# Kernel tuning notes

Hardware: AMD Instinct MI355X
Metric: run time of the kernel (lower is better)

The kernel has to match this reference:

```python
import jax, jax.numpy as jnp
import numpy as np

N_NODES = 100000
N_EDGES = 1600000
IN_DIM = 128      # 1 (degree) + 127 (raw feat)
HID = 128
N_GRAPHS = 100


def setup_inputs() -> dict:
    key = jax.random.key(0)
    ks = jax.random.split(key, 16)
    feat = jax.random.normal(ks[0], (N_NODES, IN_DIM - 1), dtype=jnp.float32)
    src = jax.random.randint(ks[1], (N_EDGES,), 0, N_NODES, dtype=jnp.int32)
    dst = jax.random.randint(ks[2], (N_EDGES,), 0, N_NODES, dtype=jnp.int32)
    graph_ids = jnp.sort(jax.random.randint(ks[3], (N_NODES,), 0, N_GRAPHS, dtype=jnp.int32))
    s = 1.0 / np.sqrt(IN_DIM)
    W0 = jax.random.uniform(ks[4], (HID, IN_DIM), jnp.float32, -s, s)
    b0 = jax.random.uniform(ks[5], (HID,), jnp.float32, -s, s)
    s = 1.0 / np.sqrt(HID)
    W1 = jax.random.uniform(ks[6], (HID, HID), jnp.float32, -s, s)
    b1 = jax.random.uniform(ks[7], (HID,), jnp.float32, -s, s)
    W2 = jax.random.uniform(ks[8], (HID, HID), jnp.float32, -s, s)
    b2 = jax.random.uniform(ks[9], (HID,), jnp.float32, -s, s)
    Wc1 = jax.random.uniform(ks[10], (HID, HID), jnp.float32, -s, s)
    bc1 = jax.random.uniform(ks[11], (HID,), jnp.float32, -s, s)
    Wc2 = jax.random.uniform(ks[12], (1, HID), jnp.float32, -s, s)
    bc2 = jax.random.uniform(ks[13], (1,), jnp.float32, -s, s)
    return {"feat": feat, "src": src, "dst": dst, "graph_ids": graph_ids,
            "num_graphs": N_GRAPHS,
            "W0": W0, "b0": b0, "W1": W1, "b1": b1, "W2": W2, "b2": b2,
            "Wc1": Wc1, "bc1": bc1, "Wc2": Wc2, "bc2": bc2}


def _gcn_layer(h, src, dst, deg, W, b):
    # mean over in-neighbor messages; zero-in-degree nodes keep old h (DGL reduce never fires)
    n = h.shape[0]
    summed = jax.ops.segment_sum(h[src], dst, num_segments=n)  # [N, d]
    mean = summed / jnp.maximum(deg, 1.0)[:, None]
    agg = jnp.where((deg > 0)[:, None], mean, h)
    return jax.nn.relu(agg @ W.T + b)


def reference(feat, src, dst, graph_ids, num_graphs,
              W0, b0, W1, b1, W2, b2, Wc1, bc1, Wc2, bc2):
    n = feat.shape[0]
    deg = jax.ops.segment_sum(jnp.ones(src.shape[0], jnp.float32), dst, num_segments=n)  # in-degrees
    h = jnp.concatenate([deg[:, None], feat], axis=-1)  # [N, IN_DIM]
    for W, b in ((W0, b0), (W1, b1), (W2, b2)):
        h = _gcn_layer(h, src, dst, deg, W, b)
    # dgl.mean_nodes: per-graph mean of node features
    counts = jax.ops.segment_sum(jnp.ones(n, jnp.float32), graph_ids, num_segments=num_graphs)
    hg = jax.ops.segment_sum(h, graph_ids, num_segments=num_graphs) / jnp.maximum(counts, 1.0)[:, None]
    # faithful: classify1 applied twice, no activation (F.relu was passed as bias flag)
    hg = hg @ Wc1.T + bc1
    hg = hg @ Wc1.T + bc1
    hg = hg @ Wc2.T + bc2
    return hg  # [num_graphs, 1]
```

## Files before the change

### kernel.cpp

```cpp
#include <hip/hip_runtime.h>
#include <hip/hip_bf16.h>

#define HID 128
#define NRAW 127
#define BSH 8
#define BNODES 256
#define EW 2048


typedef __attribute__((ext_vector_type(8))) short short8;
typedef __attribute__((ext_vector_type(4))) float floatx4;
typedef __attribute__((ext_vector_type(2))) float floatx2;

__device__ inline unsigned pack_bf2(float x, float y) {
    unsigned bx = __float_as_uint(x);
    unsigned by = __float_as_uint(y);
    bx += 0x7fffu + ((bx >> 16) & 1u);
    by += 0x7fffu + ((by >> 16) & 1u);
    return (bx >> 16) | (by & 0xffff0000u);
}
__device__ inline float bf_lo(unsigned u) { return __uint_as_float(u << 16); }
__device__ inline float bf_hi(unsigned u) { return __uint_as_float(u & 0xffff0000u); }


__global__ void init_kernel(const float* __restrict__ W0, const float* __restrict__ W1,
                            const float* __restrict__ W2, const float* __restrict__ Wc1,
                            unsigned* __restrict__ O0, unsigned* __restrict__ O1,
                            unsigned* __restrict__ O2, float* __restrict__ Wc1p,
                            int* __restrict__ gbucket, float* __restrict__ hg,
                            float* __restrict__ counts,
                            unsigned* __restrict__ h8a, unsigned* __restrict__ h8b,
                            int G, int N) {
    int id = blockIdx.x * blockDim.x + threadIdx.x;
    if (id < 512) gbucket[id] = 0;
    if (id < G * HID) hg[id] = 0.f;
    if (id < G) counts[id] = 0.f;
    if (id < 32) {
        h8a[(size_t)N * 32 + id] = 0u;
        h8b[(size_t)N * 32 + id] = 0u;
    }
    if (id < 16384) {
        int t = id >> 7, p = id & 127;
        Wc1p[id] = Wc1[t * 128 + ((p & 7) * 16 + (p >> 3))];
    }
    if (id < 3 * 8192) {
        int sel = id >> 13, l = id & 8191;
        const float* W = sel == 0 ? W0 : (sel == 1 ? W1 : W2);
        unsigned* O = sel == 0 ? O0 : (sel == 1 ? O1 : O2);
        int o = l >> 6, pp = (l & 63) * 2;
        int k0 = (pp & 7) * 16 + (pp >> 3);
        int k1 = ((pp + 1) & 7) * 16 + ((pp + 1) >> 3);
        O[l] = pack_bf2(W[o * 128 + k0], W[o * 128 + k1]);
    }
}


__global__ __launch_bounds__(256) void bucket_count_kernel(const int* __restrict__ dst,
                                                           int* __restrict__ gbucket,
                                                           int E, int NB) {
    __shared__ int hist[512];
    int t = threadIdx.x;
    for (int b = t; b < NB; b += 256) hist[b] = 0;
    __syncthreads();
    int base = blockIdx.x * 4096;
    #pragma unroll
    for (int j = 0; j < 16; ++j) {
        int e = base + j * 256 + t;
        if (e < E) atomicAdd(&hist[dst[e] >> BSH], 1);
    }
    __syncthreads();
    for (int b = t; b < NB; b += 256) {
        int v = hist[b];
        if (v) atomicAdd(&gbucket[b], v);
    }
}

__global__ void bucket_scan_kernel(const int* __restrict__ gbucket, int* __restrict__ bstart,
                                   int* __restrict__ gcur, int NB, int E) {
    __shared__ int sm[512];
    int t = threadIdx.x;
    int v = (t < NB) ? gbucket[t] : 0;
    sm[t] = v;
    __syncthreads();
    for (int off = 1; off < 512; off <<= 1) {
        int add = (t >= off) ? sm[t - off] : 0;
        __syncthreads();
        sm[t] += add;
        __syncthreads();
    }
    if (t < NB) {
        int ex = sm[t] - v;
        bstart[t] = ex;
        gcur[t] = ex;
    }
    if (t == 0) bstart[NB] = E;
}

__global__ __launch_bounds__(256) void bucket_scatter_kernel(const int* __restrict__ src,
                                                             const int* __restrict__ dst,
                                                             int* __restrict__ gcur,
                                                             unsigned* __restrict__ staging,
                                                             int E, int NB) {
    __shared__ int hist[512];
    __shared__ int base[512];
    int t = threadIdx.x;
    for (int b = t; b < NB; b += 256) hist[b] = 0;
    __syncthreads();
    int s[16], d[16], r[16];
    int e0 = blockIdx.x * 4096;
    #pragma unroll
    for (int j = 0; j < 16; ++j) {
        int e = e0 + j * 256 + t;
        if (e < E) {
            s[j] = src[e];
            d[j] = dst[e];
            r[j] = atomicAdd(&hist[d[j] >> BSH], 1);
        } else d[j] = -1;
    }
    __syncthreads();
    for (int b = t; b < NB; b += 256) {
        int v = hist[b];
        base[b] = v ? atomicAdd(&gcur[b], v) : 0;
    }
    __syncthreads();
    #pragma unroll
    for (int j = 0; j < 16; ++j) {
        if (d[j] >= 0) {
            int b = d[j] >> BSH;
            staging[base[b] + r[j]] = ((unsigned)s[j] << 8) | ((unsigned)d[j] & 255u);
        }
    }
}

__global__ __launch_bounds__(256) void csr_build_kernel(const unsigned* __restrict__ staging,
                                                        const int* __restrict__ bstart,
                                                        int* __restrict__ rp, int* __restrict__ csr,
                                                        float* __restrict__ degf,
                                                        int N, int E, int NB) {
    __shared__ int hist[256];
    __shared__ int sm[256];
    __shared__ int excl[256];
    __shared__ int cnt[256];
    int t = threadIdx.x;
    int b = blockIdx.x;
    int nbase = b << BSH;
    int s0 = bstart[b], e1 = bstart[b + 1];
    hist[t] = 0;
    __syncthreads();
    for (int i = s0 + t; i < e1; i += 256) {
        unsigned p = staging[i];
        atomicAdd(&hist[p & (BNODES - 1)], 1);
    }
    __syncthreads();
    int h = hist[t];
    sm[t] = h;
    __syncthreads();
    for (int off = 1; off < 256; off <<= 1) {
        int add = (t >= off) ? sm[t - off] : 0;
        __syncthreads();
        sm[t] += add;
        __syncthreads();
    }
    excl[t] = sm[t] - h;
    cnt[t] = 0;
    int n = nbase + t;
    if (n < N) {
        rp[n] = s0 + (sm[t] - h);
        degf[n] = (float)h;
    }
    if (b == NB - 1 && t == 0) {
        rp[N] = E;
        degf[N] = 0.f;
    }
    __syncthreads();
    for (int i = s0 + t; i < e1; i += 256) {
        unsigned p = staging[i];
        int dl = p & (BNODES - 1);
        int pos = s0 + excl[dl] + atomicAdd(&cnt[dl], 1);
        csr[pos] = (int)(p >> 8);
    }
}


__global__ __launch_bounds__(256) void build_h0_kernel(const float* __restrict__ feat,
                                                       unsigned* __restrict__ h8, int N) {
    __shared__ float lf[8 * NRAW];
    int t = threadIdx.x;
    int n0 = blockIdx.x * 8;
    int nrows = min(8, N - n0);
    int total = nrows * NRAW;
    for (int j = t; j < total; j += 256) lf[j] = feat[(size_t)n0 * NRAW + j];
    __syncthreads();
    int n = t >> 5, c = t & 31;
    if (n < nrows) {
        const float* fr = lf + n * NRAW;
        int base = c >> 1, hb = (c & 1) * 4;
        float f[4];
        #pragma unroll
        for (int j = 0; j < 4; ++j) {
            int l = (hb + j) * 16 + base;
            f[j] = (l == 0) ? 0.f : fr[l - 1];
        }
        unsigned w = __builtin_amdgcn_cvt_pk_fp8_f32(f[0], f[1], 0, false);
        w = __builtin_amdgcn_cvt_pk_fp8_f32(f[2], f[3], w, true);
        h8[(size_t)(n0 + n) * 32 + c] = w;
    }
}


__global__ __launch_bounds__(256, 4) void gcn_fused_kernel(const unsigned* __restrict__ h8,
                                                           unsigned* __restrict__ out8,
                                                           unsigned* __restrict__ outb,
                                                           const unsigned* __restrict__ Wb,
                                                           const float* __restrict__ bias,
                                                           const int* __restrict__ rp,
                                                           const int* __restrict__ csr,
                                                           const float* __restrict__ degf,
                                                           int col0fix, int N) {
    __shared__ unsigned Al[32 * 64];
    __shared__ unsigned CsS[32 * 64];
    int* sIdx = (int*)CsS;
    int t = threadIdx.x;
    int wv = t >> 6, lane = t & 63;
    int grp = lane >> 3;
    int cc4 = lane & 7;
    int n0 = blockIdx.x * 32;
    int g32 = wv * 8 + grp;
    int i = n0 + g32;
    const char* hbase = (const char*)h8;
    unsigned c16 = (unsigned)cc4 * 16u;

    int start = 0, end = 0;
    if (i < N) { start = rp[i]; end = rp[i + 1]; }
    int deg = end - start;
    int nEnd = min(n0 + 32, N);
    int s0 = rp[n0];
    int e1 = rp[nEnd];

    floatx2 a0 = {0.f, 0.f}, a1 = {0.f, 0.f}, a2 = {0.f, 0.f}, a3 = {0.f, 0.f};
    floatx2 a4 = {0.f, 0.f}, a5 = {0.f, 0.f}, a6 = {0.f, 0.f}, a7 = {0.f, 0.f};
    float dsum = 0.f;

    #define GATH4(ii) (*(const uint4*)(hbase + (((unsigned)(ii) << 7) + c16)))
    #define ACC4(vv) do { \
        a0 += __builtin_amdgcn_cvt_pk_f32_fp8((vv).x, false); \
        a1 += __builtin_amdgcn_cvt_pk_f32_fp8((vv).x, true);  \
        a2 += __builtin_amdgcn_cvt_pk_f32_fp8((vv).y, false); \
        a3 += __builtin_amdgcn_cvt_pk_f32_fp8((vv).y, true);  \
        a4 += __builtin_amdgcn_cvt_pk_f32_fp8((vv).z, false); \
        a5 += __builtin_amdgcn_cvt_pk_f32_fp8((vv).z, true);  \
        a6 += __builtin_amdgcn_cvt_pk_f32_fp8((vv).w, false); \
        a7 += __builtin_amdgcn_cvt_pk_f32_fp8((vv).w, true);  \
    } while (0)

    for (int w0 = s0; w0 < e1; w0 += EW) {
        if (w0 > s0) __syncthreads();
        int wcnt = min(EW, e1 - w0);
        for (int j = t; j < wcnt; j += 256) sIdx[j] = csr[w0 + j];
        __syncthreads();
        int p  = max(start, w0) - w0;
        int pe = min(end, w0 + wcnt) - w0;
        for (; p + 4 <= pe; p += 4) {
            int iA = sIdx[p], iB = sIdx[p + 1], iC = sIdx[p + 2], iD = sIdx[p + 3];
            uint4 vA = GATH4(iA), vB = GATH4(iB), vC = GATH4(iC), vD = GATH4(iD);
            if (col0fix && cc4 == 0)
                dsum += degf[iA] + degf[iB] + degf[iC] + degf[iD];
            ACC4(vA); ACC4(vB); ACC4(vC); ACC4(vD);
        }
        for (; p + 2 <= pe; p += 2) {
            int iA = sIdx[p], iB = sIdx[p + 1];
            uint4 vA = GATH4(iA), vB = GATH4(iB);
            if (col0fix && cc4 == 0) dsum += degf[iA] + degf[iB];
            ACC4(vA); ACC4(vB);
        }
        for (; p < pe; ++p) {
            int iA = sIdx[p];
            uint4 vA = GATH4(iA);
            if (col0fix && cc4 == 0) dsum += degf[iA];
            ACC4(vA);
        }
    }

    if (i < N) {
        float inv;
        if (deg == 0) {
            uint4 v = GATH4(i);
            ACC4(v);
            inv = 1.f;
        } else {
            if (col0fix && cc4 == 0) a0[0] = dsum;
            inv = 1.f / (float)deg;
        }
        uint4 r0, r1;
        r0.x = pack_bf2(a0[0] * inv, a0[1] * inv);
        r0.y = pack_bf2(a1[0] * inv, a1[1] * inv);
        r0.z = pack_bf2(a2[0] * inv, a2[1] * inv);
        r0.w = pack_bf2(a3[0] * inv, a3[1] * inv);
        r1.x = pack_bf2(a4[0] * inv, a4[1] * inv);
        r1.y = pack_bf2(a5[0] * inv, a5[1] * inv);
        r1.z = pack_bf2(a6[0] * inv, a6[1] * inv);
        r1.w = pack_bf2(a7[0] * inv, a7[1] * inv);
        int gr0 = 2 * cc4, gr1 = 2 * cc4 + 1;
        *(uint4*)&Al[(g32 * 16 + (gr0 ^ (g32 & 7))) * 4] = r0;
        *(uint4*)&Al[(g32 * 16 + (gr1 ^ (g32 & 7))) * 4] = r1;
    }
    __syncthreads();

    {
        int rh = wv & 1, cq = wv >> 1;
        int m = lane & 15, q = lane >> 4;
        int r = rh * 16 + m;
        floatx4 acc0 = (floatx4)(0.f), acc1 = (floatx4)(0.f);
        floatx4 acc2 = (floatx4)(0.f), acc3 = (floatx4)(0.f);
        #pragma unroll
        for (int kt = 0; kt < 4; ++kt) {
            short8 af = *(const short8*)&Al[(r * 16 + ((kt * 4 + q) ^ (m & 7))) * 4];
            short8 b0 = *(const short8*)&Wb[((cq * 4 + 0) * 16 + m) * 64 + kt * 16 + q * 4];
            short8 b1 = *(const short8*)&Wb[((cq * 4 + 1) * 16 + m) * 64 + kt * 16 + q * 4];
            short8 b2 = *(const short8*)&Wb[((cq * 4 + 2) * 16 + m) * 64 + kt * 16 + q * 4];
            short8 b3 = *(const short8*)&Wb[((cq * 4 + 3) * 16 + m) * 64 + kt * 16 + q * 4];
            acc0 = __builtin_amdgcn_mfma_f32_16x16x32_bf16(af, b0, acc0, 0, 0, 0);
            acc1 = __builtin_amdgcn_mfma_f32_16x16x32_bf16(af, b1, acc1, 0, 0, 0);
            acc2 = __builtin_amdgcn_mfma_f32_16x16x32_bf16(af, b2, acc2, 0, 0, 0);
            acc3 = __builtin_amdgcn_mfma_f32_16x16x32_bf16(af, b3, acc3, 0, 0, 0);
        }
        float bv0 = bias[(cq * 4 + 0) * 16 + m];
        float bv1 = bias[(cq * 4 + 1) * 16 + m];
        float bv2 = bias[(cq * 4 + 2) * 16 + m];
        float bv3 = bias[(cq * 4 + 3) * 16 + m];
        #pragma unroll
        for (int r4 = 0; r4 < 4; ++r4) {
            int row = rh * 16 + q * 4 + r4;
            float v0 = fmaxf(acc0[r4] + bv0, 0.f);
            float v1 = fmaxf(acc1[r4] + bv1, 0.f);
            float v2 = fmaxf(acc2[r4] + bv2, 0.f);
            float v3 = fmaxf(acc3[r4] + bv3, 0.f);
            if (out8) {
                unsigned pk = __builtin_amdgcn_cvt_pk_fp8_f32(v0, v1, 0, false);
                pk = __builtin_amdgcn_cvt_pk_fp8_f32(v2, v3, pk, true);
                *(unsigned*)((char*)CsS + row * 128 + m * 8 + cq * 4) = pk;
            } else {
                CsS[row * 64 + m * 4 + cq * 2 + 0] = pack_bf2(v0, v1);
                CsS[row * 64 + m * 4 + cq * 2 + 1] = pack_bf2(v2, v3);
            }
        }
    }
    __syncthreads();

    {
        int row = t >> 3, gg = t & 7;
        int n = n0 + row;
        if (n < N) {
            if (out8) {
                ((uint4*)out8)[(size_t)n * 8 + gg] =
                    *(const uint4*)((const char*)CsS + row * 128 + gg * 16);
            } else {
                ((uint4*)outb)[(size_t)n * 16 + 2 * gg]     = *(const uint4*)&CsS[row * 64 + 8 * gg];
                ((uint4*)outb)[(size_t)n * 16 + 2 * gg + 1] = *(const uint4*)&CsS[row * 64 + 8 * gg + 4];
            }
        }
    }
    #undef GATH4
    #undef ACC4
}


__global__ __launch_bounds__(256) void pool_kernel(const unsigned* __restrict__ h,
                                                   const int* __restrict__ gid,
                                                   float* __restrict__ hg,
                                                   float* __restrict__ counts, int N) {
    int c = threadIdx.x & 63;
    int q = threadIdx.x >> 6;
    int n0 = blockIdx.x * 64;
    int nend = min(n0 + 64, N);
    float ax = 0.f, ay = 0.f, cnt = 0.f;
    int cur = -1;
    for (int n = n0 + q; n < nend; n += 4) {
        int g = gid[n];
        if (g != cur) {
            if (cur >= 0) {
                atomicAdd(&hg[cur * HID + 2 * c], ax);
                atomicAdd(&hg[cur * HID + 2 * c + 1], ay);
                if (c == 0) atomicAdd(&counts[cur], cnt);
            }
            ax = ay = cnt = 0.f;
            cur = g;
        }
        unsigned v = h[(size_t)n * 64 + c];
        ax += bf_lo(v); ay += bf_hi(v);
        cnt += 1.f;
    }
    if (cur >= 0) {
        atomicAdd(&hg[cur * HID + 2 * c], ax);
        atomicAdd(&hg[cur * HID + 2 * c + 1], ay);
        if (c == 0) atomicAdd(&counts[cur], cnt);
    }
}


__global__ __launch_bounds__(128) void cls_fused_kernel(const float* __restrict__ hg,
                                                        const float* __restrict__ counts,
                                                        const float* __restrict__ Wc1p,
                                                        const float* __restrict__ Wc1,
                                                        const float* __restrict__ bc1,
                                                        const float* __restrict__ Wc2,
                                                        const float* __restrict__ bc2,
                                                        float* __restrict__ out, int G) {
    __shared__ float x[128];
    __shared__ float y[128];
    __shared__ float red[128];
    int g = blockIdx.x, t = threadIdx.x;
    float inv = 1.f / fmaxf(counts[g], 1.f);
    x[t] = hg[g * HID + t] * inv;
    __syncthreads();
    const float4* wp4 = (const float4*)(Wc1p + t * HID);
    float s = 0.f;
    #pragma unroll
    for (int k4 = 0; k4 < 32; ++k4) {
        float4 w = wp4[k4];
        s += x[k4 * 4] * w.x + x[k4 * 4 + 1] * w.y + x[k4 * 4 + 2] * w.z + x[k4 * 4 + 3] * w.w;
    }
    y[t] = s + bc1[t];
    __syncthreads();
    const float4* w4 = (const float4*)(Wc1 + t * HID);
    float s2 = 0.f;
    #pragma unroll
    for (int k4 = 0; k4 < 32; ++k4) {
        float4 w = w4[k4];
        s2 += y[k4 * 4] * w.x + y[k4 * 4 + 1] * w.y + y[k4 * 4 + 2] * w.z + y[k4 * 4 + 3] * w.w;
    }
    red[t] = (s2 + bc1[t]) * Wc2[t];
    __syncthreads();
    if (t < 64) {
        float r = red[t] + red[t + 64];
        #pragma unroll
        for (int off = 32; off > 0; off >>= 1) r += __shfl_down(r, off);
        if (t == 0) out[g] = r + bc2[0];
    }
}


extern "C" void kernel_launch(void* const* d_in, const int* in_sizes, int n_in,
                              void* d_out, int out_size, void* d_ws, size_t ws_size,
                              hipStream_t stream) {
    const float* feat = (const float*)d_in[0];
    const int* src    = (const int*)d_in[1];
    const int* dst    = (const int*)d_in[2];
    const int* gid    = (const int*)d_in[3];
    const float* W0  = (const float*)d_in[5];
    const float* b0  = (const float*)d_in[6];
    const float* W1  = (const float*)d_in[7];
    const float* b1  = (const float*)d_in[8];
    const float* W2  = (const float*)d_in[9];
    const float* b2  = (const float*)d_in[10];
    const float* Wc1 = (const float*)d_in[11];
    const float* bc1 = (const float*)d_in[12];
    const float* Wc2 = (const float*)d_in[13];
    const float* bc2 = (const float*)d_in[14];

    const int N = in_sizes[3];
    const int E = in_sizes[1];
    const int G = out_size;
    const int NB = (N + BNODES - 1) >> BSH;

    char* ws = (char*)d_ws;
    size_t off = 0;
    auto alloc = [&](size_t bytes) { void* p = ws + off; off += (bytes + 255) & ~size_t(255); return p; };
    unsigned* h8a    = (unsigned*)alloc((size_t)(N + 1) * 32 * 4);
    unsigned* h8b    = (unsigned*)alloc((size_t)(N + 1) * 32 * 4);
    unsigned* hB     = (unsigned*)alloc((size_t)N * 64 * 4);
    float* degf      = (float*)alloc((size_t)(N + 1) * 4);
    unsigned* staging = (unsigned*)alloc((size_t)E * 4);
    int* csr         = (int*)alloc((size_t)(E + 64) * 4);
    int* rp          = (int*)alloc((size_t)(N + 1) * 4);
    int* gbucket     = (int*)alloc(512 * 4);
    int* bstart      = (int*)alloc(513 * 4);
    int* gcur        = (int*)alloc(512 * 4);
    unsigned* Wb0    = (unsigned*)alloc(8192 * 4);
    unsigned* Wb1    = (unsigned*)alloc(8192 * 4);
    unsigned* Wb2    = (unsigned*)alloc(8192 * 4);
    float* Wc1p      = (float*)alloc(16384 * 4);
    float* hg        = (float*)alloc((size_t)G * HID * 4);
    float* counts    = (float*)alloc((size_t)G * 4);

    init_kernel<<<96, 256, 0, stream>>>(W0, W1, W2, Wc1, Wb0, Wb1, Wb2, Wc1p,
                                        gbucket, hg, counts, h8a, h8b, G, N);

    int gE = (E + 4095) / 4096;
    bucket_count_kernel<<<gE, 256, 0, stream>>>(dst, gbucket, E, NB);
    bucket_scan_kernel<<<1, 512, 0, stream>>>(gbucket, bstart, gcur, NB, E);
    bucket_scatter_kernel<<<gE, 256, 0, stream>>>(src, dst, gcur, staging, E, NB);
    csr_build_kernel<<<NB, 256, 0, stream>>>(staging, bstart, rp, csr, degf, N, E, NB);

    build_h0_kernel<<<(N + 7) / 8, 256, 0, stream>>>(feat, h8a, N);

    int layer_grid = (N + 31) / 32;
    gcn_fused_kernel<<<layer_grid, 256, 0, stream>>>(h8a, h8b, nullptr, Wb0, b0, rp, csr, degf, 1, N);
    gcn_fused_kernel<<<layer_grid, 256, 0, stream>>>(h8b, h8a, nullptr, Wb1, b1, rp, csr, degf, 0, N);
    gcn_fused_kernel<<<layer_grid, 256, 0, stream>>>(h8a, nullptr, hB, Wb2, b2, rp, csr, degf, 0, N);

    pool_kernel<<<(N + 63) / 64, 256, 0, stream>>>(hB, gid, hg, counts, N);

    cls_fused_kernel<<<G, 128, 0, stream>>>(hg, counts, Wc1p, Wc1, bc1, Wc2, bc2,
                                            (float*)d_out, G);
}
```

Measured before the change: 356.0 us.

## Replace bucketed CSR build with atomic counting sort and fuse pooling into last layer

Replaces the two-level bucketed CSR construction (bucket histogram, scan, staging scatter, per-bucket local sort) with a direct per-node atomic degree count, a three-kernel global prefix scan, and an atomic-decrement scatter into CSR. It also fuses the graph mean-pool into the final GCN layer, so the bf16 layer-3 output is no longer written to global memory and read back by a separate pool kernel. The direct scatter uses global atomics on random node addresses with uncoalesced writes, and CSR neighbor order becomes nondeterministic. The fused pool also adds atomic traffic to the per-graph sums from every layer block.

```diff
diff --git a/kernel.cpp b/kernel.cpp
--- a/kernel.cpp
+++ b/kernel.cpp
@@ -3,8 +3,6 @@
 
 #define HID 128
 #define NRAW 127
-#define BSH 8
-#define BNODES 256
 #define EW 2048
 
 
@@ -23,18 +21,20 @@
 __device__ inline float bf_hi(unsigned u) { return __uint_as_float(u & 0xffff0000u); }
 
 
-__global__ void init_kernel(const float* __restrict__ W0, const float* __restrict__ W1,
+__global__ __launch_bounds__(256) void init_kernel(const float* __restrict__ W0,
+                            const float* __restrict__ W1,
                             const float* __restrict__ W2, const float* __restrict__ Wc1,
                             unsigned* __restrict__ O0, unsigned* __restrict__ O1,
                             unsigned* __restrict__ O2, float* __restrict__ Wc1p,
-                            int* __restrict__ gbucket, float* __restrict__ hg,
-                            float* __restrict__ counts,
+                            int* __restrict__ degc, float* __restrict__ hg,
+                            float* __restrict__ counts, float* __restrict__ degf,
                             unsigned* __restrict__ h8a, unsigned* __restrict__ h8b,
                             int G, int N) {
     int id = blockIdx.x * blockDim.x + threadIdx.x;
-    if (id < 512) gbucket[id] = 0;
+    if (id < N) degc[id] = 0;
     if (id < G * HID) hg[id] = 0.f;
     if (id < G) counts[id] = 0.f;
+    if (id == 0) degf[N] = 0.f;
     if (id < 32) {
         h8a[(size_t)N * 32 + id] = 0u;
         h8b[(size_t)N * 32 + id] = 0u;
@@ -55,129 +55,71 @@
 }
 
 
-__global__ __launch_bounds__(256) void bucket_count_kernel(const int* __restrict__ dst,
-                                                           int* __restrict__ gbucket,
-                                                           int E, int NB) {
-    __shared__ int hist[512];
-    int t = threadIdx.x;
-    for (int b = t; b < NB; b += 256) hist[b] = 0;
-    __syncthreads();
-    int base = blockIdx.x * 4096;
+__global__ __launch_bounds__(256) void deg_count_kernel(const int* __restrict__ dst,
+                                                        int* __restrict__ degc, int E) {
+    int base = blockIdx.x * 4096 + threadIdx.x;
     #pragma unroll
     for (int j = 0; j < 16; ++j) {
-        int e = base + j * 256 + t;
-        if (e < E) atomicAdd(&hist[dst[e] >> BSH], 1);
-    }
-    __syncthreads();
-    for (int b = t; b < NB; b += 256) {
-        int v = hist[b];
-        if (v) atomicAdd(&gbucket[b], v);
-    }
-}
-
-__global__ void bucket_scan_kernel(const int* __restrict__ gbucket, int* __restrict__ bstart,
-                                   int* __restrict__ gcur, int NB, int E) {
-    __shared__ int sm[512];
-    int t = threadIdx.x;
-    int v = (t < NB) ? gbucket[t] : 0;
+        int e = base + j * 256;
+        if (e < E) atomicAdd(&degc[dst[e]], 1);
+    }
+}
+
+__global__ __launch_bounds__(1024) void scan1_kernel(const int* __restrict__ degc,
+                                                     int* __restrict__ rp,
+                                                     float* __restrict__ degf,
+                                                     int* __restrict__ bsum, int N) {
+    __shared__ int sm[1024];
+    int t = threadIdx.x, j = blockIdx.x * 1024 + t;
+    int v = (j < N) ? degc[j] : 0;
+    if (j < N) degf[j] = (float)v;
     sm[t] = v;
     __syncthreads();
-    for (int off = 1; off < 512; off <<= 1) {
+    for (int off = 1; off < 1024; off <<= 1) {
         int add = (t >= off) ? sm[t - off] : 0;
         __syncthreads();
         sm[t] += add;
         __syncthreads();
     }
-    if (t < NB) {
-        int ex = sm[t] - v;
-        bstart[t] = ex;
-        gcur[t] = ex;
-    }
-    if (t == 0) bstart[NB] = E;
-}
-
-__global__ __launch_bounds__(256) void bucket_scatter_kernel(const int* __restrict__ src,
-                                                             const int* __restrict__ dst,
-                                                             int* __restrict__ gcur,
-                                                             unsigned* __restrict__ staging,
-                                                             int E, int NB) {
-    __shared__ int hist[512];
-    __shared__ int base[512];
+    if (j <= N) rp[j] = sm[t] - v;
+    if (t == 1023) bsum[blockIdx.x] = sm[1023];
+}
+
+__global__ void scan2_kernel(int* __restrict__ bsum, int NS) {
+    __shared__ int sm[128];
     int t = threadIdx.x;
-    for (int b = t; b < NB; b += 256) hist[b] = 0;
-    __syncthreads();
-    int s[16], d[16], r[16];
-    int e0 = blockIdx.x * 4096;
-    #pragma unroll
-    for (int j = 0; j < 16; ++j) {
-        int e = e0 + j * 256 + t;
-        if (e < E) {
-            s[j] = src[e];
-            d[j] = dst[e];
-            r[j] = atomicAdd(&hist[d[j] >> BSH], 1);
-        } else d[j] = -1;
-    }
-    __syncthreads();
-    for (int b = t; b < NB; b += 256) {
-        int v = hist[b];
-        base[b] = v ? atomicAdd(&gcur[b], v) : 0;
-    }
-    __syncthreads();
-    #pragma unroll
-    for (int j = 0; j < 16; ++j) {
-        if (d[j] >= 0) {
-            int b = d[j] >> BSH;
-            staging[base[b] + r[j]] = ((unsigned)s[j] << 8) | ((unsigned)d[j] & 255u);
-        }
-    }
-}
-
-__global__ __launch_bounds__(256) void csr_build_kernel(const unsigned* __restrict__ staging,
-                                                        const int* __restrict__ bstart,
-                                                        int* __restrict__ rp, int* __restrict__ csr,
-                                                        float* __restrict__ degf,
-                                                        int N, int E, int NB) {
-    __shared__ int hist[256];
-    __shared__ int sm[256];
-    __shared__ int excl[256];
-    __shared__ int cnt[256];
-    int t = threadIdx.x;
-    int b = blockIdx.x;
-    int nbase = b << BSH;
-    int s0 = bstart[b], e1 = bstart[b + 1];
-    hist[t] = 0;
-    __syncthreads();
-    for (int i = s0 + t; i < e1; i += 256) {
-        unsigned p = staging[i];
-        atomicAdd(&hist[p & (BNODES - 1)], 1);
-    }
-    __syncthreads();
-    int h = hist[t];
-    sm[t] = h;
-    __syncthreads();
-    for (int off = 1; off < 256; off <<= 1) {
+    int v = (t < NS) ? bsum[t] : 0;
+    sm[t] = v;
+    __syncthreads();
+    for (int off = 1; off < 128; off <<= 1) {
         int add = (t >= off) ? sm[t - off] : 0;
         __syncthreads();
         sm[t] += add;
         __syncthreads();
     }
-    excl[t] = sm[t] - h;
-    cnt[t] = 0;
-    int n = nbase + t;
-    if (n < N) {
-        rp[n] = s0 + (sm[t] - h);
-        degf[n] = (float)h;
-    }
-    if (b == NB - 1 && t == 0) {
-        rp[N] = E;
-        degf[N] = 0.f;
-    }
-    __syncthreads();
-    for (int i = s0 + t; i < e1; i += 256) {
-        unsigned p = staging[i];
-        int dl = p & (BNODES - 1);
-        int pos = s0 + excl[dl] + atomicAdd(&cnt[dl], 1);
-        csr[pos] = (int)(p >> 8);
+    if (t < NS) bsum[t] = sm[t] - v;
+}
+
+__global__ __launch_bounds__(1024) void scan3_kernel(int* __restrict__ rp,
+                                                     const int* __restrict__ bsum, int N) {
+    int j = blockIdx.x * 1024 + threadIdx.x;
+    if (j <= N) rp[j] += bsum[blockIdx.x];
+}
+
+__global__ __launch_bounds__(256) void scatter_kernel(const int* __restrict__ src,
+                                                      const int* __restrict__ dst,
+                                                      int* __restrict__ degc,
+                                                      const int* __restrict__ rp,
+                                                      int* __restrict__ csr, int E) {
+    int base = blockIdx.x * 4096 + threadIdx.x;
+    #pragma unroll
+    for (int j = 0; j < 16; ++j) {
+        int e = base + j * 256;
+        if (e < E) {
+            int d = dst[e];
+            int o = atomicSub(&degc[d], 1);
+            csr[rp[d] + o - 1] = src[e];
+        }
     }
 }
 
@@ -210,13 +152,15 @@
 
 __global__ __launch_bounds__(256, 4) void gcn_fused_kernel(const unsigned* __restrict__ h8,
                                                            unsigned* __restrict__ out8,
-                                                           unsigned* __restrict__ outb,
                                                            const unsigned* __restrict__ Wb,
                                                            const float* __restrict__ bias,
                                                            const int* __restrict__ rp,
                                                            const int* __restrict__ csr,
                                                            const float* __restrict__ degf,
-                                                           int col0fix, int N) {
+                                                           const int* __restrict__ gid,
+                                                           float* __restrict__ hgp,
+                                                           float* __restrict__ cntp,
+                                                           int col0fix, int dopool, int N) {
     __shared__ unsigned Al[32 * 64];
     __shared__ unsigned CsS[32 * 64];
     int* sIdx = (int*)CsS;
@@ -347,54 +291,42 @@
     }
     __syncthreads();
 
-    {
+    if (dopool) {
+        int q = t >> 6, c = t & 63;
+        float ax = 0.f, ay = 0.f, cnt = 0.f;
+        int cur = -1;
+        for (int n = q; n < 32; n += 4) {
+            int nd = n0 + n;
+            if (nd >= N) break;
+            int g = gid[nd];
+            if (g != cur) {
+                if (cur >= 0) {
+                    atomicAdd(&hgp[cur * HID + 2 * c], ax);
+                    atomicAdd(&hgp[cur * HID + 2 * c + 1], ay);
+                    if (c == 0) atomicAdd(&cntp[cur], cnt);
+                }
+                ax = ay = cnt = 0.f;
+                cur = g;
+            }
+            unsigned v = CsS[n * 64 + c];
+            ax += bf_lo(v); ay += bf_hi(v);
+            cnt += 1.f;
+        }
+        if (cur >= 0) {
+            atomicAdd(&hgp[cur * HID + 2 * c], ax);
+            atomicAdd(&hgp[cur * HID + 2 * c + 1], ay);
+            if (c == 0) atomicAdd(&cntp[cur], cnt);
+        }
+    } else {
         int row = t >> 3, gg = t & 7;
         int n = n0 + row;
         if (n < N) {
-            if (out8) {
-                ((uint4*)out8)[(size_t)n * 8 + gg] =
-                    *(const uint4*)((const char*)CsS + row * 128 + gg * 16);
-            } else {
-                ((uint4*)outb)[(size_t)n * 16 + 2 * gg]     = *(const uint4*)&CsS[row * 64 + 8 * gg];
-                ((uint4*)outb)[(size_t)n * 16 + 2 * gg + 1] = *(const uint4*)&CsS[row * 64 + 8 * gg + 4];
-            }
+            ((uint4*)out8)[(size_t)n * 8 + gg] =
+                *(const uint4*)((const char*)CsS + row * 128 + gg * 16);
         }
     }
     #undef GATH4
     #undef ACC4
-}
-
-
-__global__ __launch_bounds__(256) void pool_kernel(const unsigned* __restrict__ h,
-                                                   const int* __restrict__ gid,
-                                                   float* __restrict__ hg,
-                                                   float* __restrict__ counts, int N) {
-    int c = threadIdx.x & 63;
-    int q = threadIdx.x >> 6;
-    int n0 = blockIdx.x * 64;
-    int nend = min(n0 + 64, N);
-    float ax = 0.f, ay = 0.f, cnt = 0.f;
-    int cur = -1;
-    for (int n = n0 + q; n < nend; n += 4) {
-        int g = gid[n];
-        if (g != cur) {
-            if (cur >= 0) {
-                atomicAdd(&hg[cur * HID + 2 * c], ax);
-                atomicAdd(&hg[cur * HID + 2 * c + 1], ay);
-                if (c == 0) atomicAdd(&counts[cur], cnt);
-            }
-            ax = ay = cnt = 0.f;
-            cur = g;
-        }
-        unsigned v = h[(size_t)n * 64 + c];
-        ax += bf_lo(v); ay += bf_hi(v);
-        cnt += 1.f;
-    }
-    if (cur >= 0) {
-        atomicAdd(&hg[cur * HID + 2 * c], ax);
-        atomicAdd(&hg[cur * HID + 2 * c + 1], ay);
-        if (c == 0) atomicAdd(&counts[cur], cnt);
-    }
 }
 
 
@@ -461,21 +393,17 @@
     const int N = in_sizes[3];
     const int E = in_sizes[1];
     const int G = out_size;
-    const int NB = (N + BNODES - 1) >> BSH;
 
     char* ws = (char*)d_ws;
     size_t off = 0;
     auto alloc = [&](size_t bytes) { void* p = ws + off; off += (bytes + 255) & ~size_t(255); return p; };
     unsigned* h8a    = (unsigned*)alloc((size_t)(N + 1) * 32 * 4);
     unsigned* h8b    = (unsigned*)alloc((size_t)(N + 1) * 32 * 4);
-    unsigned* hB     = (unsigned*)alloc((size_t)N * 64 * 4);
     float* degf      = (float*)alloc((size_t)(N + 1) * 4);
-    unsigned* staging = (unsigned*)alloc((size_t)E * 4);
+    int* degc        = (int*)alloc((size_t)N * 4);
     int* csr         = (int*)alloc((size_t)(E + 64) * 4);
     int* rp          = (int*)alloc((size_t)(N + 1) * 4);
-    int* gbucket     = (int*)alloc(512 * 4);
-    int* bstart      = (int*)alloc(513 * 4);
-    int* gcur        = (int*)alloc(512 * 4);
+    int* bsum        = (int*)alloc(512 * 4);
     unsigned* Wb0    = (unsigned*)alloc(8192 * 4);
     unsigned* Wb1    = (unsigned*)alloc(8192 * 4);
     unsigned* Wb2    = (unsigned*)alloc(8192 * 4);
@@ -483,23 +411,27 @@
     float* hg        = (float*)alloc((size_t)G * HID * 4);
     float* counts    = (float*)alloc((size_t)G * 4);
 
-    init_kernel<<<96, 256, 0, stream>>>(W0, W1, W2, Wc1, Wb0, Wb1, Wb2, Wc1p,
-                                        gbucket, hg, counts, h8a, h8b, G, N);
+    int initg = (N + 255) / 256;
+    init_kernel<<<initg, 256, 0, stream>>>(W0, W1, W2, Wc1, Wb0, Wb1, Wb2, Wc1p,
+                                           degc, hg, counts, degf, h8a, h8b, G, N);
 
     int gE = (E + 4095) / 4096;
-    bucket_count_kernel<<<gE, 256, 0, stream>>>(dst, gbucket, E, NB);
-    bucket_scan_kernel<<<1, 512, 0, stream>>>(gbucket, bstart, gcur, NB, E);
-    bucket_scatter_kernel<<<gE, 256, 0, stream>>>(src, dst, gcur, staging, E, NB);
-    csr_build_kernel<<<NB, 256, 0, stream>>>(staging, bstart, rp, csr, degf, N, E, NB);
+    int NS = (N + 1 + 1023) / 1024;
+    deg_count_kernel<<<gE, 256, 0, stream>>>(dst, degc, E);
+    scan1_kernel<<<NS, 1024, 0, stream>>>(degc, rp, degf, bsum, N);
+    scan2_kernel<<<1, 128, 0, stream>>>(bsum, NS);
+    scan3_kernel<<<NS, 1024, 0, stream>>>(rp, bsum, N);
+    scatter_kernel<<<gE, 256, 0, stream>>>(src, dst, degc, rp, csr, E);
 
     build_h0_kernel<<<(N + 7) / 8, 256, 0, stream>>>(feat, h8a, N);
 
     int layer_grid = (N + 31) / 32;
-    gcn_fused_kernel<<<layer_grid, 256, 0, stream>>>(h8a, h8b, nullptr, Wb0, b0, rp, csr, degf, 1, N);
-    gcn_fused_kernel<<<layer_grid, 256, 0, stream>>>(h8b, h8a, nullptr, Wb1, b1, rp, csr, degf, 0, N);
-    gcn_fused_kernel<<<layer_grid, 256, 0, stream>>>(h8a, nullptr, hB, Wb2, b2, rp, csr, degf, 0, N);
-
-    pool_kernel<<<(N + 63) / 64, 256, 0, stream>>>(hB, gid, hg, counts, N);
+    gcn_fused_kernel<<<layer_grid, 256, 0, stream>>>(h8a, h8b, Wb0, b0, rp, csr, degf,
+                                                     nullptr, nullptr, nullptr, 1, 0, N);
+    gcn_fused_kernel<<<layer_grid, 256, 0, stream>>>(h8b, h8a, Wb1, b1, rp, csr, degf,
+                                                     nullptr, nullptr, nullptr, 0, 0, N);
+    gcn_fused_kernel<<<layer_grid, 256, 0, stream>>>(h8a, nullptr, Wb2, b2, rp, csr, degf,
+                                                     gid, hg, counts, 0, 1, N);
 
     cls_fused_kernel<<<G, 128, 0, stream>>>(hg, counts, Wc1p, Wc1, bc1, Wc2, bc2,
                                             (float*)d_out, G);
```

Result: slower. 481.6 us (+35.3%).
